# Kernel optimization log

Hardware: AMD Instinct MI355X
Metric: run time of the kernel (lower is better)

The kernel has to match this reference:

```python
import jax, jax.numpy as jnp
import numpy as np

NORMAL_WEIGHT = 0.001
B, C, N = 8, 6, 4096  # N == n_samples, so no subsampling branch


def setup_inputs() -> dict:
    key = jax.random.key(0)
    k1, k2 = jax.random.split(key)
    a = jax.random.normal(k1, (B, C, N), dtype=jnp.float32)
    b = jax.random.normal(k2, (B, C, N), dtype=jnp.float32)
    return {"a": a, "b": b}


def _chamfer_with_normals(a, b):
    # a, b: [B, 6, N] -> [B, N, 6]
    at = jnp.swapaxes(a, 1, 2)
    bt = jnp.swapaxes(b, 1, 2)
    ap, an = at[:, :, 0:3], at[:, :, 3:6]  # points / normals [B,N,3]
    bp, bn = bt[:, :, 0:3], bt[:, :, 3:6]
    # batch pairwise squared distances: pd[b,i,j] = ||ap_i - bp_j||^2
    aa = jnp.sum(ap * ap, axis=-1)  # [B,N]
    bb = jnp.sum(bp * bp, axis=-1)  # [B,N]
    ab = jnp.einsum('bic,bjc->bij', ap, bp)  # [B,N,N]
    pd = aa[:, :, None] + bb[:, None, :] - 2.0 * ab
    # Faithful to torch: mma[b,i,j]=a_normals[j], mmb[b,i,j]=b_normals[i]
    # so d_norm[b,i,j] = 1 - dot(b_normals[i], a_normals[j])
    d_norm = 1.0 - jnp.einsum('bic,bjc->bij', bn, an)  # [B,N,N]
    d = pd + NORMAL_WEIGHT * d_norm
    chamfer_sym = jnp.sum(jnp.min(d, axis=2)) + jnp.sum(jnp.min(d, axis=1))
    return chamfer_sym / a.shape[0]


def reference(a, b):
    return _chamfer_with_normals(a, b)
```

## Files before the change

### kernel.cpp

```cpp
#include <hip/hip_runtime.h>


constexpr int   NPTS  = 4096;
constexpr int   CPB   = 6;
constexpr int   BATCH = 8;
constexpr float W     = 0.001f;

typedef _Float16 f16x8 __attribute__((ext_vector_type(8)));
typedef float    f32x4 __attribute__((ext_vector_type(4)));

#define MFMA32(A_, B_, C_) __builtin_amdgcn_mfma_f32_16x16x32_f16((A_), (B_), (C_), 0, 0, 0)

__device__ inline void fsplit(float x, _Float16& h, _Float16& l) {
    h = (_Float16)x;
    l = (_Float16)(x - (float)h);
}

template<int CTRL>
__device__ inline float minror(float v) {
    int s = __float_as_int(v);
    int r = __builtin_amdgcn_update_dpp(s, s, CTRL, 0xF, 0xF, false);
    return fminf(v, __int_as_float(r));
}

__global__ __launch_bounds__(256, 4) void chamfer_fused_kernel(
    const float* __restrict__ A, const float* __restrict__ B,
    float* __restrict__ partial, float* __restrict__ out)
{
    const int dir = blockIdx.z, batch = blockIdx.y, bd = dir * BATCH + batch;
    const int rg = blockIdx.x >> 3, s = blockIdx.x & 7;
    const int tid = threadIdx.x, w = tid >> 6, lane = tid & 63;
    const int quad = lane >> 4, l16 = lane & 15;
    const float* rowPos = dir ? B : A;
    const float* rowNrm = dir ? A : B;
    const float* colPos = dir ? A : B;
    const float* colNrm = dir ? B : A;
    const int bb = batch * CPB * NPTS;
    const _Float16 one = (_Float16)1.f, zz = (_Float16)0.f;

    if (blockIdx.x == 0 && blockIdx.y == 0 && blockIdx.z == 0 && tid == 0)
        out[0] = 0.f;

    __shared__ alignas(16) _Float16 lds[4 * 512 * 8];

#pragma unroll
    for (int p = 0; p < 2; ++p) {
        const int j  = p * 256 + tid;
        const int cj = s * 512 + j;
        const float q0 = colPos[bb + 0*NPTS + cj], q1 = colPos[bb + 1*NPTS + cj],
                    q2 = colPos[bb + 2*NPTS + cj];
        const float n0 = colNrm[bb + 3*NPTS + cj], n1 = colNrm[bb + 4*NPTS + cj],
                    n2 = colNrm[bb + 5*NPTS + cj];
        const float c6[6] = {q0, q1, q2, n0, n1, n2};
        const float bias = fmaf(q0, q0, fmaf(q1, q1, q2*q2)) + W;
        _Float16 ch[6], cl[6], bh, bl;
#pragma unroll
        for (int c = 0; c < 6; ++c) fsplit(c6[c], ch[c], cl[c]);
        fsplit(bias, bh, bl);
        f16x8 v0 = {ch[0], ch[1], ch[2], ch[3], ch[4], ch[5], ch[0], ch[1]};
        f16x8 v1 = {ch[2], ch[3], ch[4], ch[5], cl[0], cl[1], cl[2], cl[3]};
        f16x8 v2 = {cl[4], cl[5], cl[0], cl[1], cl[2], cl[3], cl[4], cl[5]};
        f16x8 v3 = {bh, bl, one, one, zz, zz, zz, zz};
        *(f16x8*)&lds[0 * 4096 + j * 8] = v0;
        *(f16x8*)&lds[1 * 4096 + j * 8] = v1;
        *(f16x8*)&lds[2 * 4096 + j * 8] = v2;
        *(f16x8*)&lds[3 * 4096 + j * 8] = v3;
    }

    f16x8 a[8];
#pragma unroll
    for (int rt = 0; rt < 8; ++rt) {
        const int row = rg * 512 + (w * 8 + rt) * 16 + l16;
        const float p0 = rowPos[bb + 0*NPTS + row], p1 = rowPos[bb + 1*NPTS + row],
                    p2 = rowPos[bb + 2*NPTS + row];
        const float rn0 = rowNrm[bb + 3*NPTS + row], rn1 = rowNrm[bb + 4*NPTS + row],
                    rn2 = rowNrm[bb + 5*NPTS + row];
        const float r6[6] = {-2.f*p0, -2.f*p1, -2.f*p2, -W*rn0, -W*rn1, -W*rn2};
        const float aa = fmaf(p0, p0, fmaf(p1, p1, p2*p2));
        _Float16 rh[6], rl[6], ah, al;
#pragma unroll
        for (int c = 0; c < 6; ++c) fsplit(r6[c], rh[c], rl[c]);
        fsplit(aa, ah, al);
        f16x8 af;
        if (quad == 0)      af = f16x8{rh[0], rh[1], rh[2], rh[3], rh[4], rh[5], rl[0], rl[1]};
        else if (quad == 1) af = f16x8{rl[2], rl[3], rl[4], rl[5], rh[0], rh[1], rh[2], rh[3]};
        else if (quad == 2) af = f16x8{rh[4], rh[5], rl[0], rl[1], rl[2], rl[3], rl[4], rl[5]};
        else                af = f16x8{one, one, ah, al, zz, zz, zz, zz};
        a[rt] = af;
    }

    float m[8][4];
#pragma unroll
    for (int rt = 0; rt < 8; ++rt)
#pragma unroll
        for (int r_ = 0; r_ < 4; ++r_) m[rt][r_] = 3.4e38f;

    __syncthreads();

    const _Float16* lq = &lds[quad * 4096];
    const f32x4 z = {0.f, 0.f, 0.f, 0.f};
    for (int ct = 0; ct < 32; ct += 2) {
        const f16x8 b0 = *(const f16x8*)&lq[(ct * 16 + l16) * 8];
        const f16x8 b1 = *(const f16x8*)&lq[((ct + 1) * 16 + l16) * 8];
#pragma unroll
        for (int rt = 0; rt < 8; ++rt) {
            f32x4 acc0 = MFMA32(a[rt], b0, z);
            f32x4 acc1 = MFMA32(a[rt], b1, z);
#pragma unroll
            for (int r_ = 0; r_ < 4; ++r_)
                m[rt][r_] = fminf(m[rt][r_], fminf(acc0[r_], acc1[r_]));
        }
    }

#pragma unroll
    for (int rt = 0; rt < 8; ++rt)
#pragma unroll
        for (int r_ = 0; r_ < 4; ++r_) {
            float v = m[rt][r_];
            v = minror<0x121>(v);
            v = minror<0x122>(v);
            v = minror<0x124>(v);
            v = minror<0x128>(v);
            m[rt][r_] = v;
        }
    if (l16 == 0) {
        float* pb = partial + (size_t)(s * 16 + bd) * NPTS + rg * 512;
#pragma unroll
        for (int rt = 0; rt < 8; ++rt)
            *(float4*)(pb + (w * 8 + rt) * 16 + quad * 4) =
                make_float4(m[rt][0], m[rt][1], m[rt][2], m[rt][3]);
    }
}

__global__ __launch_bounds__(256) void reduce_kernel(
    const float* __restrict__ partial, float* __restrict__ out)
{
    const int g = blockIdx.x * 256 + threadIdx.x;
    const int bd = g >> 12, row = g & (NPTS - 1);
    float v = partial[(size_t)(0 * 16 + bd) * NPTS + row];
#pragma unroll
    for (int s = 1; s < 8; ++s)
        v = fminf(v, partial[(size_t)(s * 16 + bd) * NPTS + row]);
    for (int off = 32; off; off >>= 1)
        v += __shfl_down(v, off, 64);
    __shared__ float sred[4];
    if ((threadIdx.x & 63) == 0) sred[threadIdx.x >> 6] = v;
    __syncthreads();
    if (threadIdx.x == 0)
        atomicAdd(out, (sred[0] + sred[1] + sred[2] + sred[3]) * 0.125f);
}

extern "C" void kernel_launch(void* const* d_in, const int* in_sizes, int n_in,
                              void* d_out, int out_size, void* d_ws, size_t ws_size,
                              hipStream_t stream) {
    const float* A = (const float*)d_in[0];
    const float* B = (const float*)d_in[1];
    float* out     = (float*)d_out;
    float* partial = (float*)d_ws;

    chamfer_fused_kernel<<<dim3(64, BATCH, 2), 256, 0, stream>>>(A, B, partial, out);
    reduce_kernel<<<dim3(2 * BATCH * NPTS / 256), 256, 0, stream>>>(partial, out);
}
```

Before: 79.35 us.

## Precompute split-f16 row/column records in a prep kernel, batch MFMAs before min

Adds a prep kernel that converts points and normals once into packed hi/lo f16 MFMA operand records for rows and columns in workspace. The main kernel then loads these records directly with vector copies instead of redoing the strided loads and splitting in every block, which removes the 8x redundant column conversion and the 8x redundant row conversion. The inner loop is fully unrolled and issues four MFMA pairs before the min reductions to expose more MFMA latency hiding. This costs an extra kernel launch and a global round trip of about 8 MB of packed data.

```diff
diff --git a/kernel.cpp b/kernel.cpp
--- a/kernel.cpp
+++ b/kernel.cpp
@@ -23,36 +23,49 @@
     return fminf(v, __int_as_float(r));
 }
 
-__global__ __launch_bounds__(256, 4) void chamfer_fused_kernel(
+__global__ __launch_bounds__(256) void prep_kernel(
     const float* __restrict__ A, const float* __restrict__ B,
-    float* __restrict__ partial, float* __restrict__ out)
+    _Float16* __restrict__ rowrec, _Float16* __restrict__ colpack,
+    float* __restrict__ out)
 {
-    const int dir = blockIdx.z, batch = blockIdx.y, bd = dir * BATCH + batch;
-    const int rg = blockIdx.x >> 3, s = blockIdx.x & 7;
-    const int tid = threadIdx.x, w = tid >> 6, lane = tid & 63;
-    const int quad = lane >> 4, l16 = lane & 15;
+    const int g = blockIdx.x * 256 + threadIdx.x;
+    if (g == 0) out[0] = 0.f;
+    const int j = g & (NPTS - 1), bd = g >> 12, dir = bd >> 3, batch = bd & 7;
+    const int bb = batch * CPB * NPTS;
     const float* rowPos = dir ? B : A;
     const float* rowNrm = dir ? A : B;
     const float* colPos = dir ? A : B;
     const float* colNrm = dir ? B : A;
-    const int bb = batch * CPB * NPTS;
     const _Float16 one = (_Float16)1.f, zz = (_Float16)0.f;
 
-    if (blockIdx.x == 0 && blockIdx.y == 0 && blockIdx.z == 0 && tid == 0)
-        out[0] = 0.f;
-
-    __shared__ alignas(16) _Float16 lds[4 * 512 * 8];
-
+    {
+        const float p0 = rowPos[bb + 0*NPTS + j], p1 = rowPos[bb + 1*NPTS + j],
+                    p2 = rowPos[bb + 2*NPTS + j];
+        const float n0 = rowNrm[bb + 3*NPTS + j], n1 = rowNrm[bb + 4*NPTS + j],
+                    n2 = rowNrm[bb + 5*NPTS + j];
+        const float r6[6] = {-2.f*p0, -2.f*p1, -2.f*p2, -W*n0, -W*n1, -W*n2};
+        const float aa = fmaf(p0, p0, fmaf(p1, p1, p2*p2));
+        _Float16 rh[6], rl[6], ah, al;
 #pragma unroll
-    for (int p = 0; p < 2; ++p) {
-        const int j  = p * 256 + tid;
-        const int cj = s * 512 + j;
-        const float q0 = colPos[bb + 0*NPTS + cj], q1 = colPos[bb + 1*NPTS + cj],
-                    q2 = colPos[bb + 2*NPTS + cj];
-        const float n0 = colNrm[bb + 3*NPTS + cj], n1 = colNrm[bb + 4*NPTS + cj],
-                    n2 = colNrm[bb + 5*NPTS + cj];
-        const float c6[6] = {q0, q1, q2, n0, n1, n2};
-        const float bias = fmaf(q0, q0, fmaf(q1, q1, q2*q2)) + W;
+        for (int c = 0; c < 6; ++c) fsplit(r6[c], rh[c], rl[c]);
+        fsplit(aa, ah, al);
+        f16x8 q0 = {rh[0], rh[1], rh[2], rh[3], rh[4], rh[5], rl[0], rl[1]};
+        f16x8 q1 = {rl[2], rl[3], rl[4], rl[5], rh[0], rh[1], rh[2], rh[3]};
+        f16x8 q2 = {rh[4], rh[5], rl[0], rl[1], rl[2], rl[3], rl[4], rl[5]};
+        f16x8 q3 = {one, one, ah, al, zz, zz, zz, zz};
+        _Float16* rp = rowrec + (size_t)g * 32;
+        *(f16x8*)(rp)      = q0;
+        *(f16x8*)(rp + 8)  = q1;
+        *(f16x8*)(rp + 16) = q2;
+        *(f16x8*)(rp + 24) = q3;
+    }
+    {
+        const float q0f = colPos[bb + 0*NPTS + j], q1f = colPos[bb + 1*NPTS + j],
+                    q2f = colPos[bb + 2*NPTS + j];
+        const float n0 = colNrm[bb + 3*NPTS + j], n1 = colNrm[bb + 4*NPTS + j],
+                    n2 = colNrm[bb + 5*NPTS + j];
+        const float c6[6] = {q0f, q1f, q2f, n0, n1, n2};
+        const float bias = fmaf(q0f, q0f, fmaf(q1f, q1f, q2f*q2f)) + W;
         _Float16 ch[6], cl[6], bh, bl;
 #pragma unroll
         for (int c = 0; c < 6; ++c) fsplit(c6[c], ch[c], cl[c]);
@@ -61,32 +74,38 @@
         f16x8 v1 = {ch[2], ch[3], ch[4], ch[5], cl[0], cl[1], cl[2], cl[3]};
         f16x8 v2 = {cl[4], cl[5], cl[0], cl[1], cl[2], cl[3], cl[4], cl[5]};
         f16x8 v3 = {bh, bl, one, one, zz, zz, zz, zz};
-        *(f16x8*)&lds[0 * 4096 + j * 8] = v0;
-        *(f16x8*)&lds[1 * 4096 + j * 8] = v1;
-        *(f16x8*)&lds[2 * 4096 + j * 8] = v2;
-        *(f16x8*)&lds[3 * 4096 + j * 8] = v3;
+        _Float16* cp = colpack + (size_t)g * 32;
+        *(f16x8*)(cp)      = v0;
+        *(f16x8*)(cp + 8)  = v1;
+        *(f16x8*)(cp + 16) = v2;
+        *(f16x8*)(cp + 24) = v3;
+    }
+}
+
+__global__ __launch_bounds__(256, 4) void chamfer_mfma_kernel(
+    const _Float16* __restrict__ rowrec, const _Float16* __restrict__ colpack,
+    float* __restrict__ partial)
+{
+    const int dir = blockIdx.z, batch = blockIdx.y, bd = dir * BATCH + batch;
+    const int rg = blockIdx.x >> 3, s = blockIdx.x & 7;
+    const int tid = threadIdx.x, w = tid >> 6, lane = tid & 63;
+    const int quad = lane >> 4, l16 = lane & 15;
+
+    __shared__ alignas(16) _Float16 lds[512 * 32];
+
+    {
+        const uint4* src = (const uint4*)(colpack + ((size_t)bd * NPTS + s * 512) * 32);
+        uint4* dst = (uint4*)lds;
+#pragma unroll
+        for (int i = 0; i < 8; ++i) dst[tid + i * 256] = src[tid + i * 256];
     }
 
     f16x8 a[8];
+    {
+        const f16x8* ar = (const f16x8*)(rowrec + ((size_t)bd * NPTS + rg * 512) * 32);
 #pragma unroll
-    for (int rt = 0; rt < 8; ++rt) {
-        const int row = rg * 512 + (w * 8 + rt) * 16 + l16;
-        const float p0 = rowPos[bb + 0*NPTS + row], p1 = rowPos[bb + 1*NPTS + row],
-                    p2 = rowPos[bb + 2*NPTS + row];
-        const float rn0 = rowNrm[bb + 3*NPTS + row], rn1 = rowNrm[bb + 4*NPTS + row],
-                    rn2 = rowNrm[bb + 5*NPTS + row];
-        const float r6[6] = {-2.f*p0, -2.f*p1, -2.f*p2, -W*rn0, -W*rn1, -W*rn2};
-        const float aa = fmaf(p0, p0, fmaf(p1, p1, p2*p2));
-        _Float16 rh[6], rl[6], ah, al;
-#pragma unroll
-        for (int c = 0; c < 6; ++c) fsplit(r6[c], rh[c], rl[c]);
-        fsplit(aa, ah, al);
-        f16x8 af;
-        if (quad == 0)      af = f16x8{rh[0], rh[1], rh[2], rh[3], rh[4], rh[5], rl[0], rl[1]};
-        else if (quad == 1) af = f16x8{rl[2], rl[3], rl[4], rl[5], rh[0], rh[1], rh[2], rh[3]};
-        else if (quad == 2) af = f16x8{rh[4], rh[5], rl[0], rl[1], rl[2], rl[3], rl[4], rl[5]};
-        else                af = f16x8{one, one, ah, al, zz, zz, zz, zz};
-        a[rt] = af;
+        for (int rt = 0; rt < 8; ++rt)
+            a[rt] = ar[(size_t)((w * 8 + rt) * 16 + l16) * 4 + quad];
     }
 
     float m[8][4];
@@ -97,18 +116,28 @@
 
     __syncthreads();
 
-    const _Float16* lq = &lds[quad * 4096];
+    const f16x8* lp = (const f16x8*)lds;
     const f32x4 z = {0.f, 0.f, 0.f, 0.f};
+#pragma unroll
     for (int ct = 0; ct < 32; ct += 2) {
-        const f16x8 b0 = *(const f16x8*)&lq[(ct * 16 + l16) * 8];
-        const f16x8 b1 = *(const f16x8*)&lq[((ct + 1) * 16 + l16) * 8];
+        const f16x8 b0 = lp[(size_t)(ct * 16 + l16) * 4 + quad];
+        const f16x8 b1 = lp[(size_t)((ct + 1) * 16 + l16) * 4 + quad];
 #pragma unroll
-        for (int rt = 0; rt < 8; ++rt) {
-            f32x4 acc0 = MFMA32(a[rt], b0, z);
-            f32x4 acc1 = MFMA32(a[rt], b1, z);
+        for (int g_ = 0; g_ < 2; ++g_) {
+            f32x4 acc0[4], acc1[4];
 #pragma unroll
-            for (int r_ = 0; r_ < 4; ++r_)
-                m[rt][r_] = fminf(m[rt][r_], fminf(acc0[r_], acc1[r_]));
+            for (int k = 0; k < 4; ++k) {
+                const int rt = g_ * 4 + k;
+                acc0[k] = MFMA32(a[rt], b0, z);
+                acc1[k] = MFMA32(a[rt], b1, z);
+            }
+#pragma unroll
+            for (int k = 0; k < 4; ++k) {
+                const int rt = g_ * 4 + k;
+#pragma unroll
+                for (int r_ = 0; r_ < 4; ++r_)
+                    m[rt][r_] = fminf(m[rt][r_], fminf(acc0[k][r_], acc1[k][r_]));
+            }
         }
     }
 
@@ -156,8 +185,12 @@
     const float* A = (const float*)d_in[0];
     const float* B = (const float*)d_in[1];
     float* out     = (float*)d_out;
-    float* partial = (float*)d_ws;
 
-    chamfer_fused_kernel<<<dim3(64, BATCH, 2), 256, 0, stream>>>(A, B, partial, out);
+    _Float16* rowrec  = (_Float16*)d_ws;
+    _Float16* colpack = rowrec + (size_t)2 * BATCH * NPTS * 32;
+    float*    partial = (float*)((char*)d_ws + (size_t)8 * 1024 * 1024);
+
+    prep_kernel<<<dim3(2 * BATCH * NPTS / 256), 256, 0, stream>>>(A, B, rowrec, colpack, out);
+    chamfer_mfma_kernel<<<dim3(64, BATCH, 2), 256, 0, stream>>>(rowrec, colpack, partial);
     reduce_kernel<<<dim3(2 * BATCH * NPTS / 256), 256, 0, stream>>>(partial, out);
 }
```

Measured after the change: 111.5 us. 40.5% more time.
